# Kernel tuning notes

Measured on AMD Instinct MI355X. Metric: run time of the kernel, lower is better.

The kernel has to match this reference:

```python
import jax, jax.numpy as jnp
import numpy as np

N, E, H = 20000, 640000, 128
EPS_BN = 1e-5
EPS_NORM = 1e-6


def batchnorm(x, gamma, beta):
    # BatchNorm1d in training mode: biased batch stats over dim 0
    mean = x.mean(axis=0)
    var = x.var(axis=0)
    return (x - mean) * jax.lax.rsqrt(var + EPS_BN) * gamma + beta


def setup_inputs() -> dict:
    key = jax.random.key(0)
    ks = jax.random.split(key, 10)
    s = 1.0 / np.sqrt(H)
    s3 = 1.0 / np.sqrt(3 * H)
    return {
        "edge_index": jax.random.randint(ks[0], (2, E), 0, N, dtype=jnp.int64),
        "node_features": jax.random.normal(ks[1], (N, H), dtype=jnp.float32),
        "edge_features": jax.random.normal(ks[2], (E, H), dtype=jnp.float32),
        "Wg": jax.random.uniform(ks[3], (H, 3 * H), jnp.float32, -s3, s3),
        "bg": jax.random.uniform(ks[4], (H,), jnp.float32, -s3, s3),
        "Ws": jax.random.uniform(ks[5], (H, H), jnp.float32, -s, s),
        "bs": jax.random.uniform(ks[6], (H,), jnp.float32, -s, s),
        "Wd": jax.random.uniform(ks[7], (H, H), jnp.float32, -s, s),
        "bd": jax.random.uniform(ks[8], (H,), jnp.float32, -s, s),
        "z_gamma": jnp.ones((H,), jnp.float32),
        "z_beta": jnp.zeros((H,), jnp.float32),
        "n_gamma": jnp.ones((H,), jnp.float32),
        "n_beta": jnp.zeros((H,), jnp.float32),
    }


def reference(edge_index, node_features, edge_features, Wg, bg, Ws, bs, Wd, bd,
              z_gamma, z_beta, n_gamma, n_beta):
    src = edge_index[0]
    dst = edge_index[1]
    n_nodes = node_features.shape[0]

    # edge gate: gather-concat-linear-BN-SiLU
    z = jnp.concatenate([node_features[src], node_features[dst], edge_features], axis=1)  # [E,3H]
    updated_edge = jax.nn.silu(batchnorm(z @ Wg.T + bg, z_gamma, z_beta))  # [E,H]

    # normalize edges: sigmoid, scatter-sum by src, gather back, divide
    sig = jax.nn.sigmoid(updated_edge)
    agg = jax.ops.segment_sum(sig, src, num_segments=n_nodes)  # [N,H]
    normalized = sig / (agg[src] + EPS_NORM)  # [E,H]

    # aggregate nodes: linear-gather-scale-scatter + linear
    upd_src = node_features @ Ws.T + bs  # [N,H]
    thee = (node_features @ Wd.T + bd)[dst]  # [E,H]
    upd_dst = jax.ops.segment_sum(normalized * thee, src, num_segments=n_nodes)  # [N,H]
    h = upd_src + upd_dst

    updated_nodes = node_features + jax.nn.silu(batchnorm(h, n_gamma, n_beta))
    return updated_nodes, updated_edge
```

## Files before the change

### kernel.cpp

```cpp
#include <hip/hip_runtime.h>
#include <cstddef>

#define DEVINL __device__ __forceinline__

typedef _Float16 f16;
typedef __attribute__((ext_vector_type(2))) _Float16 f16x2;
typedef __attribute__((ext_vector_type(8))) short bf16x8;
typedef __attribute__((ext_vector_type(4))) float f32x4;
typedef __attribute__((ext_vector_type(2))) float f32x2;

DEVINL unsigned short f2bf(float f) {
  unsigned int u = __builtin_bit_cast(unsigned int, f);
  u += 0x7FFFu + ((u >> 16) & 1u);
  return (unsigned short)(u >> 16);
}

DEVINL float sigm(float x) { return 1.0f / (1.0f + __expf(-x)); }

__global__ __launch_bounds__(256) void node_gemm_k(
    const float* __restrict__ nf, const float* __restrict__ Wg,
    const float* __restrict__ Ws, const float* __restrict__ bs,
    const float* __restrict__ Wd, const float* __restrict__ bd,
    f16* __restrict__ Ah, f16* __restrict__ Bh,
    float* __restrict__ S, f16* __restrict__ Dh, int N) {
  __shared__ float sNf[32 * 128];
  const int n0 = blockIdx.x * 32;
  for (int i = threadIdx.x; i < 1024; i += 256) {
    const int r = i >> 5, k = (i & 31) << 2;
    float4 v = make_float4(0.f, 0.f, 0.f, 0.f);
    if (n0 + r < N) v = *(const float4*)(nf + (size_t)(n0 + r) * 128 + k);
    *(float4*)(&sNf[r * 128 + k]) = v;
  }
  __syncthreads();
  const int c = threadIdx.x & 127, g = threadIdx.x >> 7;
  const float4* w0p = (const float4*)(Wg + (size_t)c * 384);
  const float4* w1p = (const float4*)(Wg + (size_t)c * 384 + 128);
  const float4* w2p = (const float4*)(Ws + (size_t)c * 128);
  const float4* w3p = (const float4*)(Wd + (size_t)c * 128);
  float a0[16], a1[16], a2[16], a3[16];
#pragma unroll
  for (int n = 0; n < 16; ++n) { a0[n] = 0.f; a1[n] = 0.f; a2[n] = 0.f; a3[n] = 0.f; }
#pragma unroll 4
  for (int k4 = 0; k4 < 32; ++k4) {
    const float4 w0 = w0p[k4], w1 = w1p[k4], w2 = w2p[k4], w3 = w3p[k4];
#pragma unroll
    for (int n = 0; n < 16; ++n) {
      const float4 x = *(const float4*)(&sNf[(g * 16 + n) * 128 + (k4 << 2)]);
      a0[n] += x.x * w0.x + x.y * w0.y + x.z * w0.z + x.w * w0.w;
      a1[n] += x.x * w1.x + x.y * w1.y + x.z * w1.z + x.w * w1.w;
      a2[n] += x.x * w2.x + x.y * w2.y + x.z * w2.z + x.w * w2.w;
      a3[n] += x.x * w3.x + x.y * w3.y + x.z * w3.z + x.w * w3.w;
    }
  }
  const float bsv = bs[c], bdv = bd[c];
#pragma unroll
  for (int n = 0; n < 16; ++n) {
    const int node = n0 + g * 16 + n;
    if (node < N) {
      const size_t o = (size_t)node * 128 + c;
      Ah[o] = (f16)a0[n];
      Bh[o] = (f16)a1[n];
      S[o] = a2[n] + bsv;
      Dh[o] = (f16)(a3[n] + bdv);
    }
  }
}

__global__ __launch_bounds__(256) void hist_k(const int* __restrict__ src,
                                              int* __restrict__ cnt, int E) {
  const int stride = gridDim.x * 256;
  for (int e = blockIdx.x * 256 + threadIdx.x; e < E; e += stride)
    atomicAdd(&cnt[src[e]], 1);
}

__global__ __launch_bounds__(1024) void scan_k(const int* __restrict__ cnt,
                                               int* __restrict__ off,
                                               int* __restrict__ cur, int N) {
  __shared__ int s[1024];
  const int tid = threadIdx.x;
  const int per = (N + 1023) >> 10;
  const int base = tid * per;
  int mysum = 0;
  for (int j = 0; j < per; ++j) {
    const int i = base + j;
    if (i < N) mysum += cnt[i];
  }
  s[tid] = mysum;
  __syncthreads();
  for (int d = 1; d < 1024; d <<= 1) {
    int v = 0;
    if (tid >= d) v = s[tid - d];
    __syncthreads();
    s[tid] += v;
    __syncthreads();
  }
  int run = s[tid] - mysum;
  for (int j = 0; j < per; ++j) {
    const int i = base + j;
    if (i < N) { off[i] = run; cur[i] = run; run += cnt[i]; }
  }
  if (tid == 1023) off[N] = s[1023];
}

__global__ __launch_bounds__(256) void scatter_k(const int* __restrict__ src,
                                                 int* __restrict__ cur,
                                                 int* __restrict__ list, int E) {
  const int stride = gridDim.x * 256;
  for (int e = blockIdx.x * 256 + threadIdx.x; e < E; e += stride) {
    const int p = atomicAdd(&cur[src[e]], 1);
    list[p] = e;
  }
}

template <bool L16>
__global__ __launch_bounds__(256, 4) void edge_lin_k(
    const int* __restrict__ ei, const float* __restrict__ ef,
    const float* __restrict__ Wg,
    const f16* __restrict__ Ah, const f16* __restrict__ Bh,
    f16* __restrict__ linh, float* __restrict__ linf,
    float* __restrict__ esum, float* __restrict__ esq,
    int E, int numTiles) {
  __shared__ __align__(16) short sW[128 * 136];

  const int tid = threadIdx.x;
  const int lane = tid & 63, wv = tid >> 6;
  const int l15 = lane & 15, quad = lane >> 4;
  const int r0 = wv << 4;
  const int* __restrict__ srcI = ei;
  const int* __restrict__ dstI = ei + E;

  for (int i = tid; i < 4096; i += 256) {
    const int c = i >> 5, k = (i & 31) << 2;
    const float4 v = *(const float4*)(Wg + (size_t)c * 384 + 256 + k);
    *(short4*)(&sW[c * 136 + k]) = make_short4((short)f2bf(v.x), (short)f2bf(v.y),
                                               (short)f2bf(v.z), (short)f2bf(v.w));
  }
  __syncthreads();

  float sAc[8], qAc[8];
#pragma unroll
  for (int t = 0; t < 8; ++t) { sAc[t] = 0.f; qAc[t] = 0.f; }

  for (int tile = blockIdx.x; tile < numTiles; tile += gridDim.x) {
    const int e0 = tile << 6;
    const int er = e0 + r0 + l15;
    const bool rvalid = (er < E);
    const float* __restrict__ efr = ef + (size_t)er * 128 + quad * 8;
    bf16x8 afr[4];
#pragma unroll
    for (int k0 = 0; k0 < 4; ++k0) {
      f32x4 u = (f32x4){0.f, 0.f, 0.f, 0.f}, v = (f32x4){0.f, 0.f, 0.f, 0.f};
      if (rvalid) {
        u = __builtin_nontemporal_load((const f32x4*)(efr + k0 * 32));
        v = __builtin_nontemporal_load((const f32x4*)(efr + k0 * 32 + 4));
      }
      bf16x8 a;
      a[0] = (short)f2bf(u[0]); a[1] = (short)f2bf(u[1]);
      a[2] = (short)f2bf(u[2]); a[3] = (short)f2bf(u[3]);
      a[4] = (short)f2bf(v[0]); a[5] = (short)f2bf(v[1]);
      a[6] = (short)f2bf(v[2]); a[7] = (short)f2bf(v[3]);
      afr[k0] = a;
    }

    f32x4 acc[8];
#pragma unroll
    for (int t = 0; t < 8; ++t) acc[t] = (f32x4){0.f, 0.f, 0.f, 0.f};
#pragma unroll
    for (int k0 = 0; k0 < 4; ++k0) {
#pragma unroll
      for (int t = 0; t < 8; ++t) {
        const bf16x8 b = *(const bf16x8*)(&sW[(t * 16 + l15) * 136 + k0 * 32 + quad * 8]);
        acc[t] = __builtin_amdgcn_mfma_f32_16x16x32_bf16(afr[k0], b, acc[t], 0, 0, 0);
      }
    }

#pragma unroll
    for (int i = 0; i < 4; ++i) {
      const int rl = r0 + quad * 4 + i;
      const int e = e0 + rl;
      if (e < E) {
        const int sN = srcI[e], dN = dstI[e];
        const f16* __restrict__ Ar = Ah + (size_t)sN * 128;
        const f16* __restrict__ Br = Bh + (size_t)dN * 128;
#pragma unroll
        for (int t = 0; t < 8; ++t) {
          const int c = t * 16 + l15;
          const float l = acc[t][i] + (float)Ar[c] + (float)Br[c];
          if (L16) {
            __builtin_nontemporal_store((f16)l, linh + (size_t)e * 128 + c);
          } else {
            __builtin_nontemporal_store(l, linf + (size_t)e * 128 + c);
          }
          sAc[t] += l;
          qAc[t] += l * l;
        }
      }
    }
  }

  __syncthreads();
  float* red = (float*)sW;
#pragma unroll
  for (int t = 0; t < 8; ++t) {
    float s = sAc[t], q = qAc[t];
    s += __shfl_xor(s, 16); s += __shfl_xor(s, 32);
    q += __shfl_xor(q, 16); q += __shfl_xor(q, 32);
    if (quad == 0) {
      red[wv * 128 + t * 16 + l15] = s;
      red[512 + wv * 128 + t * 16 + l15] = q;
    }
  }
  __syncthreads();
  if (tid < 128) {
    const float s = red[tid] + red[128 + tid] + red[256 + tid] + red[384 + tid];
    const float q = red[512 + tid] + red[640 + tid] + red[768 + tid] + red[896 + tid];
    unsafeAtomicAdd(&esum[tid], s);
    unsafeAtomicAdd(&esq[tid], q);
  }
}

template <bool L16>
__global__ __launch_bounds__(256) void node_agg_k(
    const f16* __restrict__ linh, float* __restrict__ outE,
    const int* __restrict__ list, const int* __restrict__ off,
    const int* __restrict__ dstI, const f16* __restrict__ Dh,
    const float* __restrict__ S,
    const float* __restrict__ esum, const float* __restrict__ esq,
    const float* __restrict__ zg, const float* __restrict__ zb, float invE,
    float* __restrict__ hvec, float* __restrict__ nsum, float* __restrict__ nsq,
    int N) {
  __shared__ float sSc[128], sSh[128];
  const int tid = threadIdx.x;
  if (tid < 128) {
    const float mean = esum[tid] * invE;
    const float var = esq[tid] * invE - mean * mean;
    const float sc = zg[tid] * rsqrtf(var + 1e-5f);
    sSc[tid] = sc;
    sSh[tid] = zb[tid] - mean * sc;
  }
  __syncthreads();

  const int lane = tid & 63, wv = tid >> 6;
  const int c0 = lane << 1;
  const int nw = gridDim.x << 2;
  const float scx = sSc[c0], scy = sSc[c0 + 1];
  const float shx = sSh[c0], shy = sSh[c0 + 1];
  float psx = 0.f, psy = 0.f, pqx = 0.f, pqy = 0.f;

  for (int n = (blockIdx.x << 2) + wv; n < N; n += nw) {
    const int o0 = off[n], o1 = off[n + 1];
    float agx = 0.f, agy = 0.f, tcx = 0.f, tcy = 0.f;
    int e = 0, d = 0;
    if (o0 < o1) { e = list[o0]; d = dstI[e]; }
    for (int i = o0; i < o1; ++i) {
      float lx, ly;
      if (L16) {
        const f16x2 u = __builtin_nontemporal_load((const f16x2*)(linh + (size_t)e * 128 + c0));
        lx = (float)u.x; ly = (float)u.y;
      } else {
        const f32x2 u = __builtin_nontemporal_load((const f32x2*)(outE + (size_t)e * 128 + c0));
        lx = u.x; ly = u.y;
      }
      const f16x2 g = *(const f16x2*)(Dh + (size_t)d * 128 + c0);
      const int ec = e;
      if (i + 1 < o1) { e = list[i + 1]; d = dstI[e]; }
      const float yx = lx * scx + shx, yy = ly * scy + shy;
      const float uex = yx * sigm(yx), uey = yy * sigm(yy);
      __builtin_nontemporal_store((f32x2){uex, uey}, (f32x2*)(outE + (size_t)ec * 128 + c0));
      const float sgx = sigm(uex), sgy = sigm(uey);
      agx += sgx; agy += sgy;
      tcx += sgx * (float)g.x; tcy += sgy * (float)g.y;
    }
    const f32x2 sv = *(const f32x2*)(S + (size_t)n * 128 + c0);
    const float hx = sv.x + tcx / (agx + 1e-6f);
    const float hy = sv.y + tcy / (agy + 1e-6f);
    __builtin_nontemporal_store((f32x2){hx, hy}, (f32x2*)(hvec + (size_t)n * 128 + c0));
    psx += hx; psy += hy;
    pqx += hx * hx; pqy += hy * hy;
  }

  __shared__ float red[1024];
  red[wv * 128 + c0] = psx;
  red[wv * 128 + c0 + 1] = psy;
  red[512 + wv * 128 + c0] = pqx;
  red[512 + wv * 128 + c0 + 1] = pqy;
  __syncthreads();
  if (tid < 128) {
    const float s = red[tid] + red[128 + tid] + red[256 + tid] + red[384 + tid];
    const float q = red[512 + tid] + red[640 + tid] + red[768 + tid] + red[896 + tid];
    unsafeAtomicAdd(&nsum[tid], s);
    unsafeAtomicAdd(&nsq[tid], q);
  }
}

__global__ __launch_bounds__(256) void node_out_k(
    const float* __restrict__ nf, const float* __restrict__ hvec,
    const float* __restrict__ nsum, const float* __restrict__ nsq,
    const float* __restrict__ ng, const float* __restrict__ nb, float invN,
    float* __restrict__ out, int total) {
  __shared__ float sSc[128], sSh[128];
  if (threadIdx.x < 128) {
    const int c = threadIdx.x;
    const float mean = nsum[c] * invN;
    const float var = nsq[c] * invN - mean * mean;
    const float sc = ng[c] * rsqrtf(var + 1e-5f);
    sSc[c] = sc;
    sSh[c] = nb[c] - mean * sc;
  }
  __syncthreads();
  const int stride = gridDim.x * 256;
  for (int idx = blockIdx.x * 256 + threadIdx.x; idx < total; idx += stride) {
    const int h = idx & 127;
    const float y = __builtin_nontemporal_load(hvec + idx) * sSc[h] + sSh[h];
    const float o = __builtin_nontemporal_load(nf + idx) + y * sigm(y);
    __builtin_nontemporal_store(o, out + idx);
  }
}

extern "C" void kernel_launch(void* const* d_in, const int* in_sizes, int n_in,
                              void* d_out, int out_size, void* d_ws, size_t ws_size,
                              hipStream_t stream) {
  const int* ei = (const int*)d_in[0];
  const float* nf = (const float*)d_in[1];
  const float* ef = (const float*)d_in[2];
  const float* Wg = (const float*)d_in[3];
  const float* Ws = (const float*)d_in[5];
  const float* bs = (const float*)d_in[6];
  const float* Wd = (const float*)d_in[7];
  const float* bd = (const float*)d_in[8];
  const float* zg = (const float*)d_in[9];
  const float* zb = (const float*)d_in[10];
  const float* ng = (const float*)d_in[11];
  const float* nb = (const float*)d_in[12];

  const int N = in_sizes[1] / 128;
  const int E = in_sizes[2] / 128;
  const size_t NH = (size_t)N * 128;

  char* p = (char*)d_ws;
  auto alloc = [&](size_t bytes) {
    char* r = p;
    p += (bytes + 255) & ~(size_t)255;
    return r;
  };
  float* S    = (float*)alloc(NH * 4);
  float* hvec = (float*)alloc(NH * 4);
  f16* Ah = (f16*)alloc(NH * 2);
  f16* Bh = (f16*)alloc(NH * 2);
  f16* Dh = (f16*)alloc(NH * 2);
  float* st = (float*)alloc(1024 * 4);
  float* esum = st;
  float* esq  = st + 128;
  float* nsum = st + 256;
  float* nsq  = st + 384;
  int* cnt  = (int*)alloc((size_t)N * 4);
  int* off  = (int*)alloc((size_t)(N + 1) * 4);
  int* cur  = (int*)alloc((size_t)N * 4);
  int* list = (int*)alloc((size_t)E * 4);
  f16* linh = (f16*)p;
  const bool L16 =
      ((size_t)(p - (char*)d_ws) + (size_t)E * 128 * 2) <= ws_size;

  float* outN = (float*)d_out;
  float* outE = outN + NH;

  hipMemsetAsync(st, 0, (size_t)((char*)cnt + (size_t)N * 4 - (char*)st), stream);

  node_gemm_k<<<(N + 31) / 32, 256, 0, stream>>>(nf, Wg, Ws, bs, Wd, bd, Ah, Bh, S, Dh, N);

  hist_k<<<640, 256, 0, stream>>>(ei, cnt, E);
  scan_k<<<1, 1024, 0, stream>>>(cnt, off, cur, N);
  scatter_k<<<640, 256, 0, stream>>>(ei, cur, list, E);

  const int numTiles = (E + 63) / 64;
  const int gblocks = numTiles < 1024 ? numTiles : 1024;
  if (L16) {
    edge_lin_k<true><<<gblocks, 256, 0, stream>>>(ei, ef, Wg, Ah, Bh, linh, nullptr,
                                                  esum, esq, E, numTiles);
    node_agg_k<true><<<(N + 3) / 4, 256, 0, stream>>>(
        linh, outE, list, off, ei + E, Dh, S, esum, esq, zg, zb, 1.0f / (float)E,
        hvec, nsum, nsq, N);
  } else {
    edge_lin_k<false><<<gblocks, 256, 0, stream>>>(ei, ef, Wg, Ah, Bh, nullptr, outE,
                                                   esum, esq, E, numTiles);
    node_agg_k<false><<<(N + 3) / 4, 256, 0, stream>>>(
        nullptr, outE, list, off, ei + E, Dh, S, esum, esq, zg, zb, 1.0f / (float)E,
        hvec, nsum, nsq, N);
  }
  node_out_k<<<640, 256, 0, stream>>>(nf, hvec, nsum, nsq, ng, nb, 1.0f / (float)N,
                                      outN, (int)NH);
}
```

Baseline: 1.160 ms.

## Process edges in CSR order and store packed edge/dst pairs for aggregation

The scatter now writes (edge id, dst) pairs plus the sorted src per CSR slot. The edge linear kernel walks edges in CSR order, so the fp16 intermediate is stored at CSR positions. The node aggregation then reads that intermediate contiguously per node instead of by random edge id, and it no longer does the indirect dst lookup. It also software-pipelines the next edge's loads. The cost is extra index storage and writes in scatter, plus gathered reads of edge features in the GEMM kernel.

```diff
diff --git a/kernel.cpp b/kernel.cpp
--- a/kernel.cpp
+++ b/kernel.cpp
@@ -97,26 +97,34 @@
   int run = s[tid] - mysum;
   for (int j = 0; j < per; ++j) {
     const int i = base + j;
-    if (i < N) { off[i] = run; cur[i] = run; run += cnt[i]; }
+    if (i < N) {
+      const int cv = cnt[i];
+      off[i] = run; cur[i] = run; run += cv;
+    }
   }
   if (tid == 1023) off[N] = s[1023];
 }
 
 __global__ __launch_bounds__(256) void scatter_k(const int* __restrict__ src,
+                                                 const int* __restrict__ dst,
                                                  int* __restrict__ cur,
-                                                 int* __restrict__ list, int E) {
+                                                 int2* __restrict__ ed,
+                                                 int* __restrict__ ssrc, int E) {
   const int stride = gridDim.x * 256;
   for (int e = blockIdx.x * 256 + threadIdx.x; e < E; e += stride) {
-    const int p = atomicAdd(&cur[src[e]], 1);
-    list[p] = e;
-  }
-}
-
-template <bool L16>
+    const int s = src[e];
+    const int p = atomicAdd(&cur[s], 1);
+    ed[p] = make_int2(e, dst[e]);
+    ssrc[p] = s;
+  }
+}
+
+template <bool CSRORD>
 __global__ __launch_bounds__(256, 4) void edge_lin_k(
     const int* __restrict__ ei, const float* __restrict__ ef,
     const float* __restrict__ Wg,
     const f16* __restrict__ Ah, const f16* __restrict__ Bh,
+    const int2* __restrict__ ed, const int* __restrict__ ssrc,
     f16* __restrict__ linh, float* __restrict__ linf,
     float* __restrict__ esum, float* __restrict__ esq,
     int E, int numTiles) {
@@ -142,10 +150,12 @@
   for (int t = 0; t < 8; ++t) { sAc[t] = 0.f; qAc[t] = 0.f; }
 
   for (int tile = blockIdx.x; tile < numTiles; tile += gridDim.x) {
-    const int e0 = tile << 6;
-    const int er = e0 + r0 + l15;
-    const bool rvalid = (er < E);
-    const float* __restrict__ efr = ef + (size_t)er * 128 + quad * 8;
+    const int p0 = tile << 6;
+    const int idxr = p0 + r0 + l15;
+    const bool rvalid = (idxr < E);
+    int erow = 0;
+    if (rvalid) erow = CSRORD ? ed[idxr].x : idxr;
+    const float* __restrict__ efr = ef + (size_t)erow * 128 + quad * 8;
     bf16x8 afr[4];
 #pragma unroll
     for (int k0 = 0; k0 < 4; ++k0) {
@@ -177,19 +187,27 @@
 #pragma unroll
     for (int i = 0; i < 4; ++i) {
       const int rl = r0 + quad * 4 + i;
-      const int e = e0 + rl;
-      if (e < E) {
-        const int sN = srcI[e], dN = dstI[e];
+      const int idx = p0 + rl;
+      if (idx < E) {
+        int sN, dN;
+        if (CSRORD) {
+          const int2 v = ed[idx];
+          dN = v.y;
+          sN = ssrc[idx];
+        } else {
+          sN = srcI[idx];
+          dN = dstI[idx];
+        }
         const f16* __restrict__ Ar = Ah + (size_t)sN * 128;
         const f16* __restrict__ Br = Bh + (size_t)dN * 128;
 #pragma unroll
         for (int t = 0; t < 8; ++t) {
           const int c = t * 16 + l15;
           const float l = acc[t][i] + (float)Ar[c] + (float)Br[c];
-          if (L16) {
-            __builtin_nontemporal_store((f16)l, linh + (size_t)e * 128 + c);
+          if (CSRORD) {
+            __builtin_nontemporal_store((f16)l, linh + (size_t)idx * 128 + c);
           } else {
-            __builtin_nontemporal_store(l, linf + (size_t)e * 128 + c);
+            __builtin_nontemporal_store(l, linf + (size_t)idx * 128 + c);
           }
           sAc[t] += l;
           qAc[t] += l * l;
@@ -219,12 +237,11 @@
   }
 }
 
-template <bool L16>
+template <bool CSRORD>
 __global__ __launch_bounds__(256) void node_agg_k(
     const f16* __restrict__ linh, float* __restrict__ outE,
-    const int* __restrict__ list, const int* __restrict__ off,
-    const int* __restrict__ dstI, const f16* __restrict__ Dh,
-    const float* __restrict__ S,
+    const int2* __restrict__ ed, const int* __restrict__ off,
+    const f16* __restrict__ Dh, const float* __restrict__ S,
     const float* __restrict__ esum, const float* __restrict__ esq,
     const float* __restrict__ zg, const float* __restrict__ zb, float invE,
     float* __restrict__ hvec, float* __restrict__ nsum, float* __restrict__ nsq,
@@ -250,26 +267,43 @@
   for (int n = (blockIdx.x << 2) + wv; n < N; n += nw) {
     const int o0 = off[n], o1 = off[n + 1];
     float agx = 0.f, agy = 0.f, tcx = 0.f, tcy = 0.f;
-    int e = 0, d = 0;
-    if (o0 < o1) { e = list[o0]; d = dstI[e]; }
-    for (int i = o0; i < o1; ++i) {
-      float lx, ly;
-      if (L16) {
-        const f16x2 u = __builtin_nontemporal_load((const f16x2*)(linh + (size_t)e * 128 + c0));
+    int e = 0;
+    float lx = 0.f, ly = 0.f;
+    f16x2 g = (f16x2){(f16)0.f, (f16)0.f};
+    if (o0 < o1) {
+      const int2 v = ed[o0];
+      e = v.x;
+      if (CSRORD) {
+        const f16x2 u = __builtin_nontemporal_load((const f16x2*)(linh + (size_t)o0 * 128 + c0));
         lx = (float)u.x; ly = (float)u.y;
       } else {
-        const f32x2 u = __builtin_nontemporal_load((const f32x2*)(outE + (size_t)e * 128 + c0));
+        const f32x2 u = *(const f32x2*)(outE + (size_t)e * 128 + c0);
         lx = u.x; ly = u.y;
       }
-      const f16x2 g = *(const f16x2*)(Dh + (size_t)d * 128 + c0);
+      g = *(const f16x2*)(Dh + (size_t)v.y * 128 + c0);
+    }
+    for (int i = o0; i < o1; ++i) {
+      const float lcx = lx, lcy = ly;
+      const f16x2 gc = g;
       const int ec = e;
-      if (i + 1 < o1) { e = list[i + 1]; d = dstI[e]; }
-      const float yx = lx * scx + shx, yy = ly * scy + shy;
+      if (i + 1 < o1) {
+        const int2 v = ed[i + 1];
+        e = v.x;
+        if (CSRORD) {
+          const f16x2 u = __builtin_nontemporal_load((const f16x2*)(linh + (size_t)(i + 1) * 128 + c0));
+          lx = (float)u.x; ly = (float)u.y;
+        } else {
+          const f32x2 u = *(const f32x2*)(outE + (size_t)e * 128 + c0);
+          lx = u.x; ly = u.y;
+        }
+        g = *(const f16x2*)(Dh + (size_t)v.y * 128 + c0);
+      }
+      const float yx = lcx * scx + shx, yy = lcy * scy + shy;
       const float uex = yx * sigm(yx), uey = yy * sigm(yy);
       __builtin_nontemporal_store((f32x2){uex, uey}, (f32x2*)(outE + (size_t)ec * 128 + c0));
       const float sgx = sigm(uex), sgy = sigm(uey);
       agx += sgx; agy += sgy;
-      tcx += sgx * (float)g.x; tcy += sgy * (float)g.y;
+      tcx += sgx * (float)gc.x; tcy += sgy * (float)gc.y;
     }
     const f32x2 sv = *(const f32x2*)(S + (size_t)n * 128 + c0);
     const float hx = sv.x + tcx / (agx + 1e-6f);
@@ -356,9 +390,10 @@
   int* cnt  = (int*)alloc((size_t)N * 4);
   int* off  = (int*)alloc((size_t)(N + 1) * 4);
   int* cur  = (int*)alloc((size_t)N * 4);
-  int* list = (int*)alloc((size_t)E * 4);
+  int2* ed  = (int2*)alloc((size_t)E * 8);
+  int* ssrc = (int*)alloc((size_t)E * 4);
   f16* linh = (f16*)p;
-  const bool L16 =
+  const bool CSRORD =
       ((size_t)(p - (char*)d_ws) + (size_t)E * 128 * 2) <= ws_size;
 
   float* outN = (float*)d_out;
@@ -370,21 +405,21 @@
 
   hist_k<<<640, 256, 0, stream>>>(ei, cnt, E);
   scan_k<<<1, 1024, 0, stream>>>(cnt, off, cur, N);
-  scatter_k<<<640, 256, 0, stream>>>(ei, cur, list, E);
+  scatter_k<<<640, 256, 0, stream>>>(ei, ei + E, cur, ed, ssrc, E);
 
   const int numTiles = (E + 63) / 64;
   const int gblocks = numTiles < 1024 ? numTiles : 1024;
-  if (L16) {
-    edge_lin_k<true><<<gblocks, 256, 0, stream>>>(ei, ef, Wg, Ah, Bh, linh, nullptr,
-                                                  esum, esq, E, numTiles);
+  if (CSRORD) {
+    edge_lin_k<true><<<gblocks, 256, 0, stream>>>(ei, ef, Wg, Ah, Bh, ed, ssrc,
+                                                  linh, nullptr, esum, esq, E, numTiles);
     node_agg_k<true><<<(N + 3) / 4, 256, 0, stream>>>(
-        linh, outE, list, off, ei + E, Dh, S, esum, esq, zg, zb, 1.0f / (float)E,
+        linh, outE, ed, off, Dh, S, esum, esq, zg, zb, 1.0f / (float)E,
         hvec, nsum, nsq, N);
   } else {
-    edge_lin_k<false><<<gblocks, 256, 0, stream>>>(ei, ef, Wg, Ah, Bh, nullptr, outE,
-                                                   esum, esq, E, numTiles);
+    edge_lin_k<false><<<gblocks, 256, 0, stream>>>(ei, ef, Wg, Ah, Bh, ed, ssrc,
+                                                   nullptr, outE, esum, esq, E, numTiles);
     node_agg_k<false><<<(N + 3) / 4, 256, 0, stream>>>(
-        nullptr, outE, list, off, ei + E, Dh, S, esum, esq, zg, zb, 1.0f / (float)E,
+        nullptr, outE, ed, off, Dh, S, esum, esq, zg, zb, 1.0f / (float)E,
         hvec, nsum, nsq, N);
   }
   node_out_k<<<640, 256, 0, stream>>>(nf, hvec, nsum, nsq, ng, nb, 1.0f / (float)N,
```

After: 1.152 ms. No clear change (-0.6%).
